# Kernel tuning notes

Hardware: AMD Instinct MI355X
Metric: run time of the kernel (lower is better)

The kernel has to match this reference:

```python
import jax, jax.numpy as jnp
import numpy as np

N_NODES = 5000
N_EDGES = 40000
BATCH = 4
SEQ = 12
IN_FEAT = 64
OUT_FEAT = 64


def setup_inputs() -> dict:
    key = jax.random.key(0)
    k1, k2, k3, k4 = jax.random.split(key, 4)
    features = jax.random.normal(k1, (N_NODES, BATCH, SEQ, IN_FEAT), dtype=jnp.float32)
    # glorot-uniform-like scale for the shared weight
    limit = np.sqrt(6.0 / (IN_FEAT + OUT_FEAT)).astype(np.float32)
    weight = jax.random.uniform(k2, (IN_FEAT, OUT_FEAT), dtype=jnp.float32,
                                minval=-limit, maxval=limit)
    edges_dst = jax.random.randint(k3, (N_EDGES,), 0, N_NODES, dtype=jnp.int32)
    edges_src = jax.random.randint(k4, (N_EDGES,), 0, N_NODES, dtype=jnp.int32)
    return {"features": features, "weight": weight,
            "edges_dst": edges_dst, "edges_src": edges_src}


def reference(features, weight, edges_dst, edges_src):
    num_nodes = features.shape[0]
    # nodes' own representation: (N, B, T, Fin) @ (Fin, Fout)
    nodes_rep = jnp.matmul(features, weight)
    # gather source-node features for every edge: (E, B, T, Fin)
    gathered = features[edges_src]
    # unsorted_segment_mean over destination nodes
    summed = jax.ops.segment_sum(gathered, edges_dst, num_segments=num_nodes)
    counts = jax.ops.segment_sum(jnp.ones((edges_dst.shape[0],), dtype=features.dtype),
                                 edges_dst, num_segments=num_nodes)
    mean = summed / jnp.maximum(counts, 1.0)[:, None, None, None]
    agg_messages = jnp.matmul(mean, weight)
    # combination_type = 'concat', activation = relu
    h = jnp.concatenate([nodes_rep, agg_messages], axis=-1)
    return jax.nn.relu(h)
```

## Files before the change

kernel.cpp:

```cpp
#include <hip/hip_runtime.h>

#define N_NODES 5000
#define N_EDGES 40000
#define ROWS 48
#define FIN 64
#define FOUT 64
#define NODE_ELEMS (ROWS * FIN)
#define OUT_ROW 128
#define NODE_OUT (ROWS * OUT_ROW)
#define CAP 64
#define M_ROWS (N_NODES * ROWS)

typedef float f32x4 __attribute__((ext_vector_type(4)));
typedef short bf16x8 __attribute__((ext_vector_type(8)));

__device__ __forceinline__ unsigned short f32_to_bf16_rne(float f) {
    unsigned int u = __float_as_uint(f);
    u += 0x7fffu + ((u >> 16) & 1u);
    return (unsigned short)(u >> 16);
}


__global__ void zero_counts_kernel(int* __restrict__ counts) {
    int i = blockIdx.x * 256 + threadIdx.x;
    if (i < N_NODES) counts[i] = 0;
}

__global__ void bucket_kernel(const int* __restrict__ edges_dst,
                              const int* __restrict__ edges_src,
                              int* __restrict__ counts,
                              int* __restrict__ bucket) {
    int e = blockIdx.x * 256 + threadIdx.x;
    if (e < N_EDGES) {
        int d = edges_dst[e];
        int slot = atomicAdd(&counts[d], 1);
        if (slot < CAP) bucket[d * CAP + slot] = edges_src[e];
    }
}


__global__ __launch_bounds__(256) void mfma_matmul_kernel(
    const float* __restrict__ feat,
    const float* __restrict__ W,
    float* __restrict__ out,
    unsigned short* __restrict__ Q) {
    __shared__ __align__(16) unsigned short a_lds[64 * 64];

    const int tid  = threadIdx.x;
    const int wave = tid >> 6;
    const int lane = tid & 63;
    const int row16 = lane & 15;
    const int koct  = lane >> 4;

    const size_t g0 = (size_t)blockIdx.x * 64;

    {
        const f32x4* src = (const f32x4*)(feat + g0 * FIN);
        #pragma unroll
        for (int i = 0; i < 4; ++i) {
            int c = tid + i * 256;
            f32x4 v = src[c];
            int r    = c >> 4;
            int kg   = (c & 15) >> 1;
            int half = c & 1;
            unsigned short p0 = f32_to_bf16_rne(v.x);
            unsigned short p1 = f32_to_bf16_rne(v.y);
            unsigned short p2 = f32_to_bf16_rne(v.z);
            unsigned short p3 = f32_to_bf16_rne(v.w);
            int us = r * 64 + ((kg ^ (r & 7)) << 3) + half * 4;
            ushort4 pk; pk.x = p0; pk.y = p1; pk.z = p2; pk.w = p3;
            *(ushort4*)(a_lds + us) = pk;
        }
    }

    bf16x8 bfrag[2][4];
    #pragma unroll
    for (int s = 0; s < 2; ++s) {
        #pragma unroll
        for (int t = 0; t < 4; ++t) {
            bf16x8 b;
            #pragma unroll
            for (int m = 0; m < 8; ++m) {
                int k = s * 32 + koct * 8 + m;
                b[m] = (short)f32_to_bf16_rne(W[k * 64 + t * 16 + row16]);
            }
            bfrag[s][t] = b;
        }
    }

    f32x4 acc[4];
    #pragma unroll
    for (int t = 0; t < 4; ++t) acc[t] = (f32x4){0.f, 0.f, 0.f, 0.f};

    __syncthreads();

    #pragma unroll
    for (int s = 0; s < 2; ++s) {
        int r  = wave * 16 + row16;
        int kg = s * 4 + koct;
        int us = r * 64 + ((kg ^ (r & 7)) << 3);
        bf16x8 a = *(const bf16x8*)(a_lds + us);
        #pragma unroll
        for (int t = 0; t < 4; ++t)
            acc[t] = __builtin_amdgcn_mfma_f32_16x16x32_bf16(a, bfrag[s][t], acc[t], 0, 0, 0);
    }

    #pragma unroll
    for (int t = 0; t < 4; ++t) {
        #pragma unroll
        for (int p = 0; p < 4; ++p) {
            size_t g = g0 + wave * 16 + koct * 4 + p;
            int col = t * 16 + row16;
            float v = acc[t][p];
            out[g * OUT_ROW + col] = fmaxf(v, 0.f);
            Q[g * FIN + col] = f32_to_bf16_rne(v);
        }
    }
}


__device__ __forceinline__ void acc_u4(float* a, uint4 v) {
    a[0] += __uint_as_float(v.x << 16); a[1] += __uint_as_float(v.x & 0xffff0000u);
    a[2] += __uint_as_float(v.y << 16); a[3] += __uint_as_float(v.y & 0xffff0000u);
    a[4] += __uint_as_float(v.z << 16); a[5] += __uint_as_float(v.z & 0xffff0000u);
    a[6] += __uint_as_float(v.w << 16); a[7] += __uint_as_float(v.w & 0xffff0000u);
}

__global__ __launch_bounds__(384) void gather_kernel(
    const unsigned short* __restrict__ Q,
    const int* __restrict__ counts,
    const int* __restrict__ bucket,
    float* __restrict__ out) {
    const int n = blockIdx.x;
    const int tid = threadIdx.x;
    const int cnt_true = counts[n];
    const int cnt = cnt_true < CAP ? cnt_true : CAP;
    const int* bk = bucket + n * CAP;

    float acc[8];
    #pragma unroll
    for (int i = 0; i < 8; ++i) acc[i] = 0.f;

    int e = 0;
    for (; e + 4 <= cnt; e += 4) {
        const unsigned short* q0 = Q + (size_t)bk[e]     * NODE_ELEMS;
        const unsigned short* q1 = Q + (size_t)bk[e + 1] * NODE_ELEMS;
        const unsigned short* q2 = Q + (size_t)bk[e + 2] * NODE_ELEMS;
        const unsigned short* q3 = Q + (size_t)bk[e + 3] * NODE_ELEMS;
        uint4 a0 = *(const uint4*)(q0 + tid * 8);
        uint4 a1 = *(const uint4*)(q1 + tid * 8);
        uint4 a2 = *(const uint4*)(q2 + tid * 8);
        uint4 a3 = *(const uint4*)(q3 + tid * 8);
        acc_u4(acc, a0); acc_u4(acc, a1); acc_u4(acc, a2); acc_u4(acc, a3);
    }
    for (; e < cnt; ++e) {
        const unsigned short* q0 = Q + (size_t)bk[e] * NODE_ELEMS;
        uint4 a0 = *(const uint4*)(q0 + tid * 8);
        acc_u4(acc, a0);
    }

    const float inv = 1.0f / (float)(cnt_true > 1 ? cnt_true : 1);
    float* outn = out + (size_t)n * NODE_OUT;

    int r = tid >> 3, c = (tid & 7) * 8;
    float* p = outn + r * OUT_ROW + 64 + c;
    f32x4 v0 = {fmaxf(acc[0] * inv, 0.f), fmaxf(acc[1] * inv, 0.f),
                fmaxf(acc[2] * inv, 0.f), fmaxf(acc[3] * inv, 0.f)};
    f32x4 v1 = {fmaxf(acc[4] * inv, 0.f), fmaxf(acc[5] * inv, 0.f),
                fmaxf(acc[6] * inv, 0.f), fmaxf(acc[7] * inv, 0.f)};
    *(f32x4*)(p)     = v0;
    *(f32x4*)(p + 4) = v1;
}


__global__ void hist_kernel(const int* __restrict__ edges_dst, int* __restrict__ counts) {
    int e = blockIdx.x * 256 + threadIdx.x;
    if (e < N_EDGES) atomicAdd(&counts[edges_dst[e]], 1);
}

__global__ void scan_kernel(const int* __restrict__ counts,
                            int* __restrict__ offsets,
                            int* __restrict__ cursor) {
    __shared__ int buf[1024];
    __shared__ int carry_s;
    int tid = threadIdx.x;
    if (tid == 0) carry_s = 0;
    __syncthreads();
    for (int base = 0; base < N_NODES; base += 1024) {
        int i = base + tid;
        int v = (i < N_NODES) ? counts[i] : 0;
        buf[tid] = v;
        __syncthreads();
        int x = v;
        for (int off = 1; off < 1024; off <<= 1) {
            int t = (tid >= off) ? buf[tid - off] : 0;
            __syncthreads();
            x += t;
            buf[tid] = x;
            __syncthreads();
        }
        int c = carry_s;
        if (i < N_NODES) {
            int excl = c + x - v;
            offsets[i] = excl;
            cursor[i] = excl;
        }
        __syncthreads();
        if (tid == 0) carry_s = c + buf[1023];
        __syncthreads();
    }
    if (threadIdx.x == 0) offsets[N_NODES] = carry_s;
}

__global__ void scatter_kernel(const int* __restrict__ edges_dst,
                               const int* __restrict__ edges_src,
                               int* __restrict__ cursor,
                               int* __restrict__ csr_src) {
    int e = blockIdx.x * 256 + threadIdx.x;
    if (e < N_EDGES) {
        int d = edges_dst[e];
        int p = atomicAdd(&cursor[d], 1);
        csr_src[p] = edges_src[e];
    }
}

__global__ __launch_bounds__(256) void fused_kernel(
    const float* __restrict__ feat,
    const float* __restrict__ W,
    const int* __restrict__ offsets,
    const int* __restrict__ csr_src,
    float* __restrict__ out) {
    __shared__ __align__(16) float lds_w[FIN * FOUT];
    __shared__ __align__(16) float lds_t[NODE_ELEMS];

    const int n = blockIdx.x;
    const int tid = threadIdx.x;

    {
        const f32x4* w4 = (const f32x4*)W;
        f32x4* l4 = (f32x4*)lds_w;
        #pragma unroll
        for (int i = 0; i < 4; ++i) l4[tid + i * 256] = w4[tid + i * 256];
    }
    {
        const f32x4* f4 = (const f32x4*)(feat + (size_t)n * NODE_ELEMS);
        f32x4* l4 = (f32x4*)lds_t;
        #pragma unroll
        for (int i = 0; i < 3; ++i) l4[tid + i * 256] = f4[tid + i * 256];
    }
    __syncthreads();

    const int j = tid & 63;
    float wcol[64];
    #pragma unroll
    for (int k = 0; k < 64; ++k) wcol[k] = lds_w[k * 64 + j];

    float* outn = out + (size_t)n * NODE_OUT;

    #pragma unroll
    for (int i = 0; i < 12; ++i) {
        int r = (tid + i * 256) >> 6;
        const f32x4* m4 = (const f32x4*)(lds_t + r * 64);
        float s = 0.f;
        #pragma unroll
        for (int k4 = 0; k4 < 16; ++k4) {
            f32x4 m = m4[k4];
            s += m.x * wcol[4 * k4 + 0] + m.y * wcol[4 * k4 + 1] +
                 m.z * wcol[4 * k4 + 2] + m.w * wcol[4 * k4 + 3];
        }
        outn[r * OUT_ROW + j] = fmaxf(s, 0.f);
    }

    const int e0 = offsets[n], e1 = offsets[n + 1];
    f32x4 acc[3];
    #pragma unroll
    for (int i = 0; i < 3; ++i) acc[i] = (f32x4){0.f, 0.f, 0.f, 0.f};
    for (int e = e0; e < e1; ++e) {
        int src = csr_src[e];
        const f32x4* f4 = (const f32x4*)(feat + (size_t)src * NODE_ELEMS);
        #pragma unroll
        for (int i = 0; i < 3; ++i) acc[i] += f4[tid + i * 256];
    }
    const float inv = 1.0f / (float)((e1 - e0) > 1 ? (e1 - e0) : 1);

    __syncthreads();
    {
        f32x4* l4 = (f32x4*)lds_t;
        #pragma unroll
        for (int i = 0; i < 3; ++i) l4[tid + i * 256] = acc[i] * inv;
    }
    __syncthreads();

    #pragma unroll
    for (int i = 0; i < 12; ++i) {
        int r = (tid + i * 256) >> 6;
        const f32x4* m4 = (const f32x4*)(lds_t + r * 64);
        float s = 0.f;
        #pragma unroll
        for (int k4 = 0; k4 < 16; ++k4) {
            f32x4 m = m4[k4];
            s += m.x * wcol[4 * k4 + 0] + m.y * wcol[4 * k4 + 1] +
                 m.z * wcol[4 * k4 + 2] + m.w * wcol[4 * k4 + 3];
        }
        outn[r * OUT_ROW + 64 + j] = fmaxf(s, 0.f);
    }
}


extern "C" void kernel_launch(void* const* d_in, const int* in_sizes, int n_in,
                              void* d_out, int out_size, void* d_ws, size_t ws_size,
                              hipStream_t stream) {
    const float* feat = (const float*)d_in[0];
    const float* W    = (const float*)d_in[1];
    const int* edst   = (const int*)d_in[2];
    const int* esrc   = (const int*)d_in[3];
    float* out = (float*)d_out;

    int* counts  = (int*)d_ws;
    int* bucket  = (int*)((char*)d_ws + 20480);
    const size_t q_off = 20480 + (size_t)N_NODES * CAP * 4;
    unsigned short* Q = (unsigned short*)((char*)d_ws + q_off);
    const size_t q_bytes = (size_t)N_NODES * NODE_ELEMS * 2;

    if (ws_size >= q_off + q_bytes) {
        zero_counts_kernel<<<(N_NODES + 255) / 256, 256, 0, stream>>>(counts);
        bucket_kernel<<<(N_EDGES + 255) / 256, 256, 0, stream>>>(edst, esrc, counts, bucket);
        mfma_matmul_kernel<<<M_ROWS / 64, 256, 0, stream>>>(feat, W, out, Q);
        gather_kernel<<<N_NODES, 384, 0, stream>>>(Q, counts, bucket, out);
    } else {
        int* offsets = counts + N_NODES;
        int* cursor  = offsets + N_NODES + 1;
        int* csr_src = cursor + N_NODES;
        zero_counts_kernel<<<(N_NODES + 255) / 256, 256, 0, stream>>>(counts);
        hist_kernel<<<(N_EDGES + 255) / 256, 256, 0, stream>>>(edst, counts);
        scan_kernel<<<1, 1024, 0, stream>>>(counts, offsets, cursor);
        scatter_kernel<<<(N_EDGES + 255) / 256, 256, 0, stream>>>(edst, esrc, cursor, csr_src);
        fused_kernel<<<N_NODES, 256, 0, stream>>>(feat, W, offsets, csr_src, out);
    }
}
```

Measured before the change: 80.00 us.

## Pre-transpose weight to bf16 and stage matmul output through LDS

Adds a prep kernel that zeroes the counts and also writes a transposed bf16 copy of the weight, so each matmul block loads its B fragments as 16-byte vectors instead of doing strided scalar loads and conversions. A fragments now go straight from global memory into registers, which removes the LDS staging and barrier before the MFMAs. The accumulators are written to an fp32 LDS tile and then stored to the output and to Q with coalesced vector writes, replacing the scattered scalar stores. In exchange the matmul needs 16KB of LDS and a barrier after the MFMAs, and the workspace layout shifts by 8KB.

```diff
diff --git a/kernel.cpp b/kernel.cpp
--- a/kernel.cpp
+++ b/kernel.cpp
@@ -21,9 +21,30 @@
 }
 
 
-__global__ void zero_counts_kernel(int* __restrict__ counts) {
-    int i = blockIdx.x * 256 + threadIdx.x;
-    if (i < N_NODES) counts[i] = 0;
+__global__ void prep_kernel(const float* __restrict__ W,
+                            int* __restrict__ counts,
+                            unsigned short* __restrict__ Wt) {
+    const int tid = threadIdx.x;
+    if (blockIdx.x < 20) {
+        int i = blockIdx.x * 256 + tid;
+        if (i < N_NODES) counts[i] = 0;
+    } else {
+        int base = tid * 16;
+        int j = base >> 6;
+        int k0 = base & 63;
+        ushort4 pk[4];
+        #pragma unroll
+        for (int q = 0; q < 4; ++q) {
+            unsigned short p[4];
+            #pragma unroll
+            for (int m = 0; m < 4; ++m)
+                p[m] = f32_to_bf16_rne(W[(k0 + q * 4 + m) * 64 + j]);
+            pk[q].x = p[0]; pk[q].y = p[1]; pk[q].z = p[2]; pk[q].w = p[3];
+        }
+        #pragma unroll
+        for (int q = 0; q < 4; ++q)
+            *(ushort4*)(Wt + j * 64 + k0 + q * 4) = pk[q];
+    }
 }
 
 __global__ void bucket_kernel(const int* __restrict__ edges_dst,
@@ -41,10 +62,10 @@
 
 __global__ __launch_bounds__(256) void mfma_matmul_kernel(
     const float* __restrict__ feat,
-    const float* __restrict__ W,
+    const unsigned short* __restrict__ Wt,
     float* __restrict__ out,
     unsigned short* __restrict__ Q) {
-    __shared__ __align__(16) unsigned short a_lds[64 * 64];
+    __shared__ __align__(16) float c_lds[64 * 64];
 
     const int tid  = threadIdx.x;
     const int wave = tid >> 6;
@@ -54,67 +75,74 @@
 
     const size_t g0 = (size_t)blockIdx.x * 64;
 
+    const float* arow = feat + (g0 + wave * 16 + row16) * FIN + koct * 8;
+    f32x4 a00 = *(const f32x4*)(arow);
+    f32x4 a01 = *(const f32x4*)(arow + 4);
+    f32x4 a10 = *(const f32x4*)(arow + 32);
+    f32x4 a11 = *(const f32x4*)(arow + 36);
+
+    bf16x8 bfrag[2][4];
+    #pragma unroll
+    for (int t = 0; t < 4; ++t) {
+        const unsigned short* wcol = Wt + (t * 16 + row16) * 64 + koct * 8;
+        bfrag[0][t] = *(const bf16x8*)(wcol);
+        bfrag[1][t] = *(const bf16x8*)(wcol + 32);
+    }
+
+    bf16x8 afrag[2];
     {
-        const f32x4* src = (const f32x4*)(feat + g0 * FIN);
-        #pragma unroll
-        for (int i = 0; i < 4; ++i) {
-            int c = tid + i * 256;
-            f32x4 v = src[c];
-            int r    = c >> 4;
-            int kg   = (c & 15) >> 1;
-            int half = c & 1;
-            unsigned short p0 = f32_to_bf16_rne(v.x);
-            unsigned short p1 = f32_to_bf16_rne(v.y);
-            unsigned short p2 = f32_to_bf16_rne(v.z);
-            unsigned short p3 = f32_to_bf16_rne(v.w);
-            int us = r * 64 + ((kg ^ (r & 7)) << 3) + half * 4;
-            ushort4 pk; pk.x = p0; pk.y = p1; pk.z = p2; pk.w = p3;
-            *(ushort4*)(a_lds + us) = pk;
-        }
-    }
-
-    bf16x8 bfrag[2][4];
-    #pragma unroll
-    for (int s = 0; s < 2; ++s) {
-        #pragma unroll
-        for (int t = 0; t < 4; ++t) {
-            bf16x8 b;
-            #pragma unroll
-            for (int m = 0; m < 8; ++m) {
-                int k = s * 32 + koct * 8 + m;
-                b[m] = (short)f32_to_bf16_rne(W[k * 64 + t * 16 + row16]);
-            }
-            bfrag[s][t] = b;
-        }
+        unsigned short p[16];
+        #pragma unroll
+        for (int m = 0; m < 4; ++m) {
+            p[m]      = f32_to_bf16_rne(a00[m]);
+            p[4 + m]  = f32_to_bf16_rne(a01[m]);
+            p[8 + m]  = f32_to_bf16_rne(a10[m]);
+            p[12 + m] = f32_to_bf16_rne(a11[m]);
+        }
+        #pragma unroll
+        for (int m = 0; m < 8; ++m) { afrag[0][m] = (short)p[m]; afrag[1][m] = (short)p[8 + m]; }
     }
 
     f32x4 acc[4];
     #pragma unroll
     for (int t = 0; t < 4; ++t) acc[t] = (f32x4){0.f, 0.f, 0.f, 0.f};
 
-    __syncthreads();
-
-    #pragma unroll
-    for (int s = 0; s < 2; ++s) {
-        int r  = wave * 16 + row16;
-        int kg = s * 4 + koct;
-        int us = r * 64 + ((kg ^ (r & 7)) << 3);
-        bf16x8 a = *(const bf16x8*)(a_lds + us);
+    #pragma unroll
+    for (int s = 0; s < 2; ++s)
         #pragma unroll
         for (int t = 0; t < 4; ++t)
-            acc[t] = __builtin_amdgcn_mfma_f32_16x16x32_bf16(a, bfrag[s][t], acc[t], 0, 0, 0);
-    }
-
-    #pragma unroll
-    for (int t = 0; t < 4; ++t) {
-        #pragma unroll
-        for (int p = 0; p < 4; ++p) {
-            size_t g = g0 + wave * 16 + koct * 4 + p;
-            int col = t * 16 + row16;
-            float v = acc[t][p];
-            out[g * OUT_ROW + col] = fmaxf(v, 0.f);
-            Q[g * FIN + col] = f32_to_bf16_rne(v);
-        }
+            acc[t] = __builtin_amdgcn_mfma_f32_16x16x32_bf16(afrag[s], bfrag[s][t], acc[t], 0, 0, 0);
+
+    #pragma unroll
+    for (int t = 0; t < 4; ++t)
+        #pragma unroll
+        for (int p = 0; p < 4; ++p)
+            c_lds[(wave * 16 + koct * 4 + p) * 64 + t * 16 + row16] = acc[t][p];
+    __syncthreads();
+
+    #pragma unroll
+    for (int i = 0; i < 4; ++i) {
+        int c = tid + i * 256;
+        int r = c >> 4;
+        int cq = c & 15;
+        f32x4 v = ((const f32x4*)c_lds)[c];
+        f32x4 rv = {fmaxf(v.x, 0.f), fmaxf(v.y, 0.f), fmaxf(v.z, 0.f), fmaxf(v.w, 0.f)};
+        *(f32x4*)(out + (g0 + r) * OUT_ROW + cq * 4) = rv;
+    }
+    #pragma unroll
+    for (int i = 0; i < 2; ++i) {
+        int c = tid + i * 256;
+        int r = c >> 3;
+        int part = c & 7;
+        const float* src = c_lds + r * 64 + part * 8;
+        ushort4 lo, hi;
+        lo.x = f32_to_bf16_rne(src[0]); lo.y = f32_to_bf16_rne(src[1]);
+        lo.z = f32_to_bf16_rne(src[2]); lo.w = f32_to_bf16_rne(src[3]);
+        hi.x = f32_to_bf16_rne(src[4]); hi.y = f32_to_bf16_rne(src[5]);
+        hi.z = f32_to_bf16_rne(src[6]); hi.w = f32_to_bf16_rne(src[7]);
+        unsigned short* dst = Q + (g0 + r) * FIN + part * 8;
+        *(ushort4*)(dst) = lo;
+        *(ushort4*)(dst + 4) = hi;
     }
 }
 
@@ -172,6 +200,11 @@
     *(f32x4*)(p + 4) = v1;
 }
 
+
+__global__ void zero_counts_kernel(int* __restrict__ counts) {
+    int i = blockIdx.x * 256 + threadIdx.x;
+    if (i < N_NODES) counts[i] = 0;
+}
 
 __global__ void hist_kernel(const int* __restrict__ edges_dst, int* __restrict__ counts) {
     int e = blockIdx.x * 256 + threadIdx.x;
@@ -318,14 +351,16 @@
 
     int* counts  = (int*)d_ws;
     int* bucket  = (int*)((char*)d_ws + 20480);
-    const size_t q_off = 20480 + (size_t)N_NODES * CAP * 4;
+    const size_t wt_off = 20480 + (size_t)N_NODES * CAP * 4;
+    unsigned short* Wt = (unsigned short*)((char*)d_ws + wt_off);
+    const size_t q_off = wt_off + 8192;
     unsigned short* Q = (unsigned short*)((char*)d_ws + q_off);
     const size_t q_bytes = (size_t)N_NODES * NODE_ELEMS * 2;
 
     if (ws_size >= q_off + q_bytes) {
-        zero_counts_kernel<<<(N_NODES + 255) / 256, 256, 0, stream>>>(counts);
+        prep_kernel<<<21, 256, 0, stream>>>(W, counts, Wt);
         bucket_kernel<<<(N_EDGES + 255) / 256, 256, 0, stream>>>(edst, esrc, counts, bucket);
-        mfma_matmul_kernel<<<M_ROWS / 64, 256, 0, stream>>>(feat, W, out, Q);
+        mfma_matmul_kernel<<<M_ROWS / 64, 256, 0, stream>>>(feat, Wt, out, Q);
         gather_kernel<<<N_NODES, 384, 0, stream>>>(Q, counts, bucket, out);
     } else {
         int* offsets = counts + N_NODES;
```

New measurement: 82.16 us. +2.7%, slower.
